# Kernel tuning notes

Measured on AMD Instinct MI355X. Metric: run time of the kernel, lower is better.

## Reference

```python
import jax, jax.numpy as jnp
import numpy as np

EPS = 1e-3  # keras BatchNormalization default epsilon

def hard_sigmoid(x):
    # keras ConvLSTM default recurrent_activation
    return jnp.clip(0.2 * x + 0.5, 0.0, 1.0)

def conv1d(x, w):
    # x: [N, L, Cin], w: [K, Cin, Cout], stride 1, SAME padding
    return jax.lax.conv_general_dilated(x, w, (1,), 'SAME',
                                        dimension_numbers=('NWC', 'WIO', 'NWC'))

def convlstm1d(x, Wx, Wh, b):
    # x: [B, T, L, Cin]; Wx: [3, Cin, 4F]; Wh: [3, F, 4F]; b: [4F]
    # Keras gate order along last axis: i, f, c, o; activation='relu'.
    B, T, L, Cin = x.shape
    F = Wh.shape[1]
    # precompute input-to-gate convs for all timesteps at once
    xg = conv1d(x.reshape(B * T, L, Cin), Wx).reshape(B, T, L, 4 * F) + b

    def step(carry, xg_t):
        h, c = carry  # [B, L, F] each
        g = xg_t + conv1d(h, Wh)          # [B, L, 4F]
        i, f, cg, o = jnp.split(g, 4, axis=-1)
        c = hard_sigmoid(f) * c + hard_sigmoid(i) * jax.nn.relu(cg)
        h = hard_sigmoid(o) * jax.nn.relu(c)
        return (h, c), h

    h0 = jnp.zeros((B, L, F), x.dtype)
    _, hs = jax.lax.scan(step, (h0, h0), jnp.moveaxis(xg, 1, 0))
    return jnp.moveaxis(hs, 0, 1)  # [B, T, L, F]

def bn(x, g, be, m, v):
    # inference-mode BatchNormalization over last (channel) axis
    return (x - m) * jax.lax.rsqrt(v + EPS) * g + be

def setup_inputs() -> dict:
    key = jax.random.key(0)
    ks = iter(jax.random.split(key, 40))
    B, T, L = 32, 32, 128
    F1, F2, F3 = 64, 128, 256
    def w(shape, s=0.05):
        return (s * jax.random.normal(next(ks), shape)).astype(jnp.float32)
    def bn_params(c):
        return (jnp.ones((c,), jnp.float32) + w((c,)), w((c,)),
                w((c,)), jnp.ones((c,), jnp.float32))
    d = {'x': jax.random.normal(next(ks), (B, T, L), jnp.float32)}
    d['Wx1'], d['Wh1'], d['b1'] = w((3, 1, 4 * F1)), w((3, F1, 4 * F1)), w((4 * F1,))
    d['Wx2'], d['Wh2'], d['b2'] = w((3, F1, 4 * F2)), w((3, F2, 4 * F2)), w((4 * F2,))
    d['Wx3'], d['Wh3'], d['b3'] = w((3, F2, 4 * F3)), w((3, F3, 4 * F3)), w((4 * F3,))
    d['g1'], d['be1'], d['m1'], d['v1'] = bn_params(F1)
    d['g2'], d['be2'], d['m2'], d['v2'] = bn_params(F2)
    d['g3'], d['be3'], d['m3'], d['v3'] = bn_params(F3)
    d['D1'], d['db1'] = w((L * F3, 1024), 0.02), w((1024,))
    d['D2'], d['db2'] = w((1024, 512), 0.02), w((512,))
    d['D3'], d['db3'] = w((512, 5), 0.02), w((5,))
    return d

def reference(x, Wx1, Wh1, b1, Wx2, Wh2, b2, Wx3, Wh3, b3,
              g1, be1, m1, v1, g2, be2, m2, v2, g3, be3, m3, v3,
              D1, db1, D2, db2, D3, db3):
    a = x[..., None]                                   # [B, T, L, 1]
    a = bn(convlstm1d(a, Wx1, Wh1, b1), g1, be1, m1, v1)   # [B, T, L, 64]
    a = bn(convlstm1d(a, Wx2, Wh2, b2), g2, be2, m2, v2)   # [B, T, L, 128]
    a = convlstm1d(a, Wx3, Wh3, b3)[:, -1]              # return_sequences=False -> [B, L, 256]
    a = bn(a, g3, be3, m3, v3)
    a = a.reshape(a.shape[0], -1)                       # [B, L*256]
    a = jax.nn.relu(a @ D1 + db1)
    a = jax.nn.relu(a @ D2 + db2)
    return jax.nn.softmax(a @ D3 + db3, axis=-1)        # [B, 5]
```

## Files before the change

### kernel.cpp

```cpp
#include <hip/hip_runtime.h>
#include <math.h>

#define BN_EPS 1e-3f

typedef unsigned short ushort;
typedef unsigned int uint;
typedef __attribute__((ext_vector_type(8))) short bf16x8;
typedef __attribute__((ext_vector_type(4))) float f32x4;

__device__ __forceinline__ float hsig(float x) {
    return fminf(fmaxf(0.2f * x + 0.5f, 0.f), 1.f);
}
__device__ __forceinline__ ushort f2bf(float f) {
    uint u = __float_as_uint(f);
    u += 0x7fffu + ((u >> 16) & 1u);
    return (ushort)(u >> 16);
}

__device__ __forceinline__ void gld_lds16(const void* g, void* l) {
    __builtin_amdgcn_global_load_lds(
        (const __attribute__((address_space(1))) void*)g,
        (__attribute__((address_space(3))) void*)l, 16, 0, 0);
}

__global__ __launch_bounds__(256)
void pack_w(const float* __restrict__ Wx, int Cin,
            const float* __restrict__ Wh, int F,
            uint4* __restrict__ wp, int S0, int S)
{
    __shared__ ushort Wt[32][136];
    const int nblk = blockIdx.x, step = blockIdx.y;
    const int tid = threadIdx.x;
    const int N4 = 4 * F;

    for (int idx = tid; idx < 32 * 128; idx += 256) {
        int kk = idx >> 7, c = idx & 127;
        int gate = c >> 5, fl = c & 31;
        int n = gate * F + nblk * 32 + fl;
        float v = 0.f;
        if (step < S0) {
            int ka = step * 32 + kk;
            if (ka < 3 * Cin) v = Wx[(long)ka * N4 + n];
        } else {
            int ka = (step - S0) * 32 + kk;
            v = Wh[(long)ka * N4 + n];
        }
        Wt[kk][c] = f2bf(v);
    }
    __syncthreads();

    for (int s = tid; s < 512; s += 256) {
        int colgrp = s >> 6, qq = (s >> 4) & 3, rr = s & 15;
        int gate = colgrp >> 1, wn = colgrp & 1;
        int c = gate * 32 + wn * 16 + rr;
        ushort tmp[8];
#pragma unroll
        for (int j = 0; j < 8; ++j) tmp[j] = Wt[qq * 8 + j][c];
        wp[(long)(nblk * S + step) * 512 + s] = *(const uint4*)tmp;
    }
}

struct GateCfg {
    const void* a0;
    const ushort* h_old;
    ushort* h_new;
    const uint4* wp;
    const float* bias;
    float* c_state;
    void* bn_out;
    const float* bn_g; const float* bn_b; const float* bn_m; const float* bn_v;
    long a0_bs;
    long bn_bs;
    int C0, S0, S, F;
    int nf_log2;
    int cin1;
    int bnf32;
    int active;
};

__global__ __launch_bounds__(256)
void gate_diag(GateCfg c3, GateCfg c2, GateCfg c1, int L)
{
    constexpr int ASLOTS = 256;
    constexpr int BSLOTS = 512;

    __shared__ __align__(16) ushort As[2][ASLOTS * 8];
    __shared__ __align__(16) ushort Bs[2][BSLOTS * 8];

    GateCfg c; int tile;
    const int bid = blockIdx.x;
    if (bid < 512)      { c = c3; tile = bid; }
    else if (bid < 768) { c = c2; tile = bid - 512; }
    else                { c = c1; tile = bid - 768; }
    if (!c.active) return;

    const int fblk = tile & ((1 << c.nf_log2) - 1);
    const int rest = tile >> c.nf_log2;
    const int lblk = rest & 1;
    const int b = rest >> 1;

    const int tid = threadIdx.x;
    const int lane = tid & 63;
    const int wave = tid >> 6;
    const int wn = wave & 1, wm = wave >> 1;
    const int q = lane >> 4, r = lane & 15;
    const int f0 = fblk * 32;
    const int l0 = lblk * 64;
    const int F = c.F;
    const int c0shift = 31 - __clz(c.C0 > 0 ? c.C0 : 1);
    const int cFshift = 31 - __clz(F);
    const int S = c.S, S0 = c.S0;

    const int mtile = tid >> 6, within = tid & 63;
    const int qq = within >> 4, rr = within & 15;
    const int row = mtile * 16 + rr;
    const int base_l = l0 + row - 1;

    const ushort* a0p = (const ushort*)c.a0 + (long)b * c.a0_bs
                        + ((long)base_l << c0shift) + qq * 8;
    const ushort* hp  = c.h_old + ((long)b * L + base_l) * F + qq * 8;
    const uint4*  wpB = c.wp + (long)fblk * S * BSLOTS;

    auto a_fetch = [&](int step, uint4& out) {
        out = uint4{0u, 0u, 0u, 0u};
        if (c.cin1 && step < S0) {
            if (qq == 0) {
                const float* xb = (const float*)c.a0 + (long)b * c.a0_bs;
                ushort t[8] = {0, 0, 0, 0, 0, 0, 0, 0};
#pragma unroll
                for (int j = 0; j < 3; ++j) {
                    int l = base_l + j;
                    if (l >= 0 && l < L) t[j] = f2bf(xb[l]);
                }
                out = *(const uint4*)t;
            }
            return;
        }
        const ushort* p; int kb, csh;
        if (step < S0) { p = a0p; kb = step * 32;        csh = c0shift; }
        else           { p = hp;  kb = (step - S0) * 32; csh = cFshift; }
        int l = base_l + (kb >> csh);
        if ((unsigned)l < (unsigned)L) out = *(const uint4*)(p + kb);
    };

    auto b_stage = [&](int step, int bufi) {
        const uint4* src = wpB + (long)step * BSLOTS + tid;
        ushort* dst = &Bs[bufi][(tid & ~63) * 8];
#pragma unroll
        for (int j = 0; j < 2; ++j)
            gld_lds16(src + j * 256, dst + j * 256 * 8);
    };

    f32x4 acc[2][4];
#pragma unroll
    for (int mt = 0; mt < 2; ++mt)
#pragma unroll
        for (int g = 0; g < 4; ++g) acc[mt][g] = (f32x4)(0.f);

    {
        uint4 aP;
        b_stage(0, 0);
        a_fetch(0, aP);
        ((uint4*)As[0])[tid] = aP;
    }
    __syncthreads();

    for (int step = 0; step < S; ++step) {
        const int buf = step & 1;
        const int nbuf = buf ^ 1;
        const bool hasNext = (step + 1 < S);
        uint4 aN;
        if (hasNext) {
            b_stage(step + 1, nbuf);
            a_fetch(step + 1, aN);
        }

        bf16x8 af[2], bfr[4];
#pragma unroll
        for (int mt = 0; mt < 2; ++mt)
            af[mt] = *(const bf16x8*)&As[buf][((wm * 2 + mt) * 64 + lane) * 8];
#pragma unroll
        for (int g = 0; g < 4; ++g)
            bfr[g] = *(const bf16x8*)&Bs[buf][((g * 2 + wn) * 64 + lane) * 8];
#pragma unroll
        for (int mt = 0; mt < 2; ++mt)
#pragma unroll
            for (int g = 0; g < 4; ++g)
                acc[mt][g] = __builtin_amdgcn_mfma_f32_16x16x32_bf16(
                    af[mt], bfr[g], acc[mt][g], 0, 0, 0);

        if (hasNext) ((uint4*)As[nbuf])[tid] = aN;
        __syncthreads();
    }

    const int f = f0 + wn * 16 + r;
    const float b_i = c.bias[f], b_f = c.bias[F + f];
    const float b_c = c.bias[2 * F + f], b_o = c.bias[3 * F + f];
    float sc = 0.f, sh = 0.f;
    if (c.bn_out) {
        sc = c.bn_g[f] * rsqrtf(c.bn_v[f] + BN_EPS);
        sh = c.bn_b[f] - c.bn_m[f] * sc;
    }
#pragma unroll
    for (int mt = 0; mt < 2; ++mt) {
#pragma unroll
        for (int reg = 0; reg < 4; ++reg) {
            const int l = l0 + (wm * 2 + mt) * 16 + q * 4 + reg;
            const long idx = ((long)b * L + l) * F + f;
            float gi = acc[mt][0][reg] + b_i;
            float gf = acc[mt][1][reg] + b_f;
            float gc = acc[mt][2][reg] + b_c;
            float go = acc[mt][3][reg] + b_o;
            float cold = c.c_state[idx];
            float cn = hsig(gf) * cold + hsig(gi) * fmaxf(gc, 0.f);
            float hn = hsig(go) * fmaxf(cn, 0.f);
            c.c_state[idx] = cn;
            c.h_new[idx] = f2bf(hn);
            if (c.bn_out) {
                float bv = hn * sc + sh;
                if (c.bnf32)
                    ((float*)c.bn_out)[(long)b * c.bn_bs + (long)l * F + f] = bv;
                else
                    ((ushort*)c.bn_out)[(long)b * c.bn_bs + (long)l * F + f] = f2bf(bv);
            }
        }
    }
}

#define DP_FMA(kk, W) do {                                         \
    const f32x4 a0 = *(const f32x4*)&A_s[(kk) * 32 + mg * 8];      \
    const f32x4 a1 = *(const f32x4*)&A_s[(kk) * 32 + mg * 8 + 4];  \
    acc[0] += a0.x * (W); acc[1] += a0.y * (W);                    \
    acc[2] += a0.z * (W); acc[3] += a0.w * (W);                    \
    acc[4] += a1.x * (W); acc[5] += a1.y * (W);                    \
    acc[6] += a1.z * (W); acc[7] += a1.w * (W);                    \
} while (0)

__global__ __launch_bounds__(256)
void dense_partial(const float* __restrict__ A,
                   const float* __restrict__ Wt,
                   float* __restrict__ partials,
                   int K, int N)
{
    __shared__ __align__(16) float A_s[128 * 32];
    const int n0 = blockIdx.x * 256;
    const int k0 = blockIdx.y * 128;
    const int tid = threadIdx.x;

    for (int idx = tid; idx < 128 * 32; idx += 256) {
        int k = idx >> 5, m = idx & 31;
        A_s[idx] = A[(long)m * K + k0 + k];
    }
    __syncthreads();

    const int nq = (tid & 63) * 4;
    const int mg = tid >> 6;
    f32x4 acc[8];
#pragma unroll
    for (int i = 0; i < 8; ++i) acc[i] = (f32x4)(0.f);

    const float* wptr = &Wt[(long)k0 * N + n0 + nq];
    f32x4 wcur = *(const f32x4*)wptr;
    f32x4 wnx  = *(const f32x4*)(wptr + N);
    wptr += 2 * (long)N;

#pragma unroll 2
    for (int k = 0; k < 126; ++k) {
        f32x4 wnew = *(const f32x4*)wptr;
        wptr += N;
        DP_FMA(k, wcur);
        wcur = wnx; wnx = wnew;
    }
    DP_FMA(126, wcur);
    DP_FMA(127, wnx);

#pragma unroll
    for (int mm = 0; mm < 8; ++mm)
        *(f32x4*)&partials[((long)blockIdx.y * 32 + mg * 8 + mm) * N + n0 + nq] = acc[mm];
}

__global__ __launch_bounds__(256)
void dense_reduce_relu(const float* __restrict__ partials,
                       const float* __restrict__ bias,
                       float* __restrict__ out, int N, int nK)
{
    int idx = blockIdx.x * 256 + threadIdx.x;
    int m = idx / N, n = idx % N;
    float s = bias[n];
#pragma unroll 4
    for (int j = 0; j < nK; ++j) s += partials[((long)j * 32 + m) * N + n];
    out[idx] = fmaxf(s, 0.f);
}

__global__ __launch_bounds__(256)
void dense_relu(const float* __restrict__ A, const float* __restrict__ Wt,
                const float* __restrict__ bias, float* __restrict__ out,
                int K, int N)
{
    __shared__ float A_s[1024];
    int n = blockIdx.x * 256 + threadIdx.x;
    int m = blockIdx.y;
    for (int k = threadIdx.x; k < K; k += 256) A_s[k] = A[(long)m * K + k];
    __syncthreads();
    float acc = 0.f;
#pragma unroll 8
    for (int k = 0; k < K; ++k)
        acc += A_s[k] * Wt[(long)k * N + n];
    out[(long)m * N + n] = fmaxf(acc + bias[n], 0.f);
}

__global__ __launch_bounds__(64)
void dense_softmax(const float* __restrict__ A, const float* __restrict__ W,
                   const float* __restrict__ bias, float* __restrict__ out)
{
    int b = blockIdx.x;
    int tid = threadIdx.x;
    __shared__ float logits[5];

    float part[5] = {0.f, 0.f, 0.f, 0.f, 0.f};
    for (int k = tid; k < 512; k += 64) {
        float a = A[b * 512 + k];
#pragma unroll
        for (int j = 0; j < 5; ++j) part[j] += a * W[k * 5 + j];
    }
#pragma unroll
    for (int j = 0; j < 5; ++j) {
        float v = part[j];
        for (int off = 32; off; off >>= 1) v += __shfl_down(v, off);
        if (tid == 0) logits[j] = v + bias[j];
    }
    __syncthreads();
    if (tid == 0) {
        float mx = logits[0];
        for (int j = 1; j < 5; ++j) mx = fmaxf(mx, logits[j]);
        float s = 0.f, e[5];
        for (int j = 0; j < 5; ++j) { e[j] = expf(logits[j] - mx); s += e[j]; }
        for (int j = 0; j < 5; ++j) out[b * 5 + j] = e[j] / s;
    }
}

extern "C" void kernel_launch(void* const* d_in, const int* in_sizes, int n_in,
                              void* d_out, int out_size, void* d_ws, size_t ws_size,
                              hipStream_t stream)
{
    const int B = 32, T = 32, L = 128;
    const int F1 = 64, F2 = 128, F3 = 256;

    const float* x   = (const float*)d_in[0];
    const float* Wx1 = (const float*)d_in[1];
    const float* Wh1 = (const float*)d_in[2];
    const float* b1  = (const float*)d_in[3];
    const float* Wx2 = (const float*)d_in[4];
    const float* Wh2 = (const float*)d_in[5];
    const float* b2  = (const float*)d_in[6];
    const float* Wx3 = (const float*)d_in[7];
    const float* Wh3 = (const float*)d_in[8];
    const float* b3  = (const float*)d_in[9];
    const float* g1  = (const float*)d_in[10];
    const float* be1 = (const float*)d_in[11];
    const float* m1  = (const float*)d_in[12];
    const float* v1  = (const float*)d_in[13];
    const float* g2  = (const float*)d_in[14];
    const float* be2 = (const float*)d_in[15];
    const float* m2  = (const float*)d_in[16];
    const float* v2  = (const float*)d_in[17];
    const float* g3  = (const float*)d_in[18];
    const float* be3 = (const float*)d_in[19];
    const float* m3  = (const float*)d_in[20];
    const float* v3  = (const float*)d_in[21];
    const float* D1  = (const float*)d_in[22];
    const float* db1 = (const float*)d_in[23];
    const float* D2  = (const float*)d_in[24];
    const float* db2 = (const float*)d_in[25];
    const float* D3  = (const float*)d_in[26];
    const float* db3 = (const float*)d_in[27];
    (void)in_sizes; (void)n_in; (void)out_size; (void)ws_size;

    char* p = (char*)d_ws;
    ushort* h1seq = (ushort*)p; p += (size_t)B * T * L * F1 * 2;
    ushort* h2seq = (ushort*)p; p += (size_t)B * T * L * F2 * 2;
    ushort* h1a = (ushort*)p; p += (size_t)B * L * F1 * 2;
    ushort* h1b = (ushort*)p; p += (size_t)B * L * F1 * 2;
    ushort* h2a = (ushort*)p; p += (size_t)B * L * F2 * 2;
    ushort* h2b = (ushort*)p; p += (size_t)B * L * F2 * 2;
    ushort* h3a = (ushort*)p; p += (size_t)B * L * F3 * 2;
    ushort* h3b = (ushort*)p; p += (size_t)B * L * F3 * 2;
    float*  c1s = (float*)p; p += (size_t)B * L * F1 * 4;
    float*  c2s = (float*)p; p += (size_t)B * L * F2 * 4;
    float*  c3s = (float*)p; p += (size_t)B * L * F3 * 4;
    float*  h3bn = (float*)p; p += (size_t)B * L * F3 * 4;
    uint4*  wp1 = (uint4*)p; p += (size_t)2 * 7 * 512 * 16;
    uint4*  wp2 = (uint4*)p; p += (size_t)4 * 18 * 512 * 16;
    uint4*  wp3 = (uint4*)p; p += (size_t)8 * 36 * 512 * 16;
    float*  a1 = (float*)p; p += (size_t)B * 1024 * 4;
    float*  a2 = (float*)p; p += (size_t)B * 512 * 4;
    float* partials = (float*)h2seq;

    pack_w<<<dim3(2, 7), 256, 0, stream>>>(Wx1, 1, Wh1, F1, wp1, 1, 7);
    pack_w<<<dim3(4, 18), 256, 0, stream>>>(Wx2, F1, Wh2, F2, wp2, 6, 18);
    pack_w<<<dim3(8, 36), 256, 0, stream>>>(Wx3, F2, Wh3, F3, wp3, 12, 36);

    hipMemsetAsync(h1a, 0, (size_t)B * L * F1 * 2, stream);
    hipMemsetAsync(h2a, 0, (size_t)B * L * F2 * 2, stream);
    hipMemsetAsync(h3a, 0, (size_t)B * L * F3 * 2, stream);
    hipMemsetAsync(c1s, 0, (size_t)B * L * F1 * 4, stream);
    hipMemsetAsync(c2s, 0, (size_t)B * L * F2 * 4, stream);
    hipMemsetAsync(c3s, 0, (size_t)B * L * F3 * 4, stream);

    for (int d = 0; d < T + 2; ++d) {
        GateCfg c1c = {}, c2c = {}, c3c = {};

        int t1 = d;
        if (t1 >= 0 && t1 < T) {
            c1c.active = 1; c1c.cin1 = 1; c1c.bnf32 = 0;
            c1c.a0 = x + (long)t1 * L; c1c.a0_bs = (long)T * L;
            c1c.C0 = 1; c1c.S0 = 1; c1c.S = 7; c1c.F = F1; c1c.nf_log2 = 1;
            c1c.h_old = (t1 & 1) ? h1b : h1a;
            c1c.h_new = (t1 & 1) ? h1a : h1b;
            c1c.wp = wp1; c1c.bias = b1; c1c.c_state = c1s;
            c1c.bn_out = h1seq + (long)t1 * L * F1; c1c.bn_bs = (long)T * L * F1;
            c1c.bn_g = g1; c1c.bn_b = be1; c1c.bn_m = m1; c1c.bn_v = v1;
        }
        int t2 = d - 1;
        if (t2 >= 0 && t2 < T) {
            c2c.active = 1; c2c.cin1 = 0; c2c.bnf32 = 0;
            c2c.a0 = h1seq + (long)t2 * L * F1; c2c.a0_bs = (long)T * L * F1;
            c2c.C0 = F1; c2c.S0 = 6; c2c.S = 18; c2c.F = F2; c2c.nf_log2 = 2;
            c2c.h_old = (t2 & 1) ? h2b : h2a;
            c2c.h_new = (t2 & 1) ? h2a : h2b;
            c2c.wp = wp2; c2c.bias = b2; c2c.c_state = c2s;
            c2c.bn_out = h2seq + (long)t2 * L * F2; c2c.bn_bs = (long)T * L * F2;
            c2c.bn_g = g2; c2c.bn_b = be2; c2c.bn_m = m2; c2c.bn_v = v2;
        }
        int t3 = d - 2;
        if (t3 >= 0 && t3 < T) {
            c3c.active = 1; c3c.cin1 = 0; c3c.bnf32 = 1;
            c3c.a0 = h2seq + (long)t3 * L * F2; c3c.a0_bs = (long)T * L * F2;
            c3c.C0 = F2; c3c.S0 = 12; c3c.S = 36; c3c.F = F3; c3c.nf_log2 = 3;
            c3c.h_old = (t3 & 1) ? h3b : h3a;
            c3c.h_new = (t3 & 1) ? h3a : h3b;
            c3c.wp = wp3; c3c.bias = b3; c3c.c_state = c3s;
            c3c.bn_out = (t3 == T - 1) ? (void*)h3bn : nullptr;
            c3c.bn_bs = (long)L * F3;
            c3c.bn_g = g3; c3c.bn_b = be3; c3c.bn_m = m3; c3c.bn_v = v3;
        }
        gate_diag<<<896, 256, 0, stream>>>(c3c, c2c, c1c, L);
    }

    {
        const int K = L * F3;
        dense_partial<<<dim3(4, 256), 256, 0, stream>>>(h3bn, D1, partials, K, 1024);
        dense_reduce_relu<<<(B * 1024) / 256, 256, 0, stream>>>(partials, db1, a1, 1024, 256);
    }
    dense_relu<<<dim3(512 / 256, B), 256, 0, stream>>>(a1, D2, db2, a2, 1024, 512);
    dense_softmax<<<B, 64, 0, stream>>>(a2, D3, db3, (float*)d_out);
}
```

Before: 1.372 ms.

## Triple-buffer gate GEMM and load A tiles directly to LDS

```diff
diff --git a/kernel.cpp b/kernel.cpp
--- a/kernel.cpp
+++ b/kernel.cpp
@@ -79,13 +79,14 @@
 };
 
 __global__ __launch_bounds__(256)
-void gate_diag(GateCfg c3, GateCfg c2, GateCfg c1, int L)
+void gate_diag(GateCfg c3, GateCfg c2, GateCfg c1, int L,
+               const ushort* __restrict__ zbuf)
 {
     constexpr int ASLOTS = 256;
     constexpr int BSLOTS = 512;
 
-    __shared__ __align__(16) ushort As[2][ASLOTS * 8];
-    __shared__ __align__(16) ushort Bs[2][BSLOTS * 8];
+    __shared__ __align__(16) ushort As[3][ASLOTS * 8];
+    __shared__ __align__(16) ushort Bs[3][BSLOTS * 8];
 
     GateCfg c; int tile;
     const int bid = blockIdx.x;
@@ -111,9 +112,8 @@
     const int cFshift = 31 - __clz(F);
     const int S = c.S, S0 = c.S0;
 
-    const int mtile = tid >> 6, within = tid & 63;
-    const int qq = within >> 4, rr = within & 15;
-    const int row = mtile * 16 + rr;
+    const int qq = lane >> 4, rr = lane & 15;
+    const int row = wave * 16 + rr;
     const int base_l = l0 + row - 1;
 
     const ushort* a0p = (const ushort*)c.a0 + (long)b * c.a0_bs
@@ -121,59 +121,64 @@
     const ushort* hp  = c.h_old + ((long)b * L + base_l) * F + qq * 8;
     const uint4*  wpB = c.wp + (long)fblk * S * BSLOTS;
 
-    auto a_fetch = [&](int step, uint4& out) {
-        out = uint4{0u, 0u, 0u, 0u};
-        if (c.cin1 && step < S0) {
-            if (qq == 0) {
-                const float* xb = (const float*)c.a0 + (long)b * c.a0_bs;
-                ushort t[8] = {0, 0, 0, 0, 0, 0, 0, 0};
-#pragma unroll
-                for (int j = 0; j < 3; ++j) {
-                    int l = base_l + j;
-                    if (l >= 0 && l < L) t[j] = f2bf(xb[l]);
-                }
-                out = *(const uint4*)t;
-            }
-            return;
-        }
+    auto stageB = [&](int step, int bufi) {
+        const uint4* src = wpB + (long)step * BSLOTS + tid;
+        ushort* dst = &Bs[bufi][(tid & ~63) * 8];
+        gld_lds16(src, dst);
+        gld_lds16(src + 256, dst + 256 * 8);
+    };
+    auto stageA = [&](int step, int bufi) {
         const ushort* p; int kb, csh;
         if (step < S0) { p = a0p; kb = step * 32;        csh = c0shift; }
         else           { p = hp;  kb = (step - S0) * 32; csh = cFshift; }
-        int l = base_l + (kb >> csh);
-        if ((unsigned)l < (unsigned)L) out = *(const uint4*)(p + kb);
+        const int l = base_l + (kb >> csh);
+        const void* src = ((unsigned)l < (unsigned)L) ? (const void*)(p + kb)
+                                                      : (const void*)zbuf;
+        gld_lds16(src, &As[bufi][(tid & ~63) * 8]);
     };
 
-    auto b_stage = [&](int step, int bufi) {
-        const uint4* src = wpB + (long)step * BSLOTS + tid;
-        ushort* dst = &Bs[bufi][(tid & ~63) * 8];
-#pragma unroll
-        for (int j = 0; j < 2; ++j)
-            gld_lds16(src + j * 256, dst + j * 256 * 8);
-    };
-
     f32x4 acc[2][4];
 #pragma unroll
     for (int mt = 0; mt < 2; ++mt)
 #pragma unroll
         for (int g = 0; g < 4; ++g) acc[mt][g] = (f32x4)(0.f);
 
-    {
-        uint4 aP;
-        b_stage(0, 0);
-        a_fetch(0, aP);
-        ((uint4*)As[0])[tid] = aP;
-    }
-    __syncthreads();
+    if (c.cin1) {
+        uint4 a0v = {0u, 0u, 0u, 0u};
+        if (qq == 0) {
+            const float* xb = (const float*)c.a0 + (long)b * c.a0_bs;
+            ushort t[8] = {0, 0, 0, 0, 0, 0, 0, 0};
+#pragma unroll
+            for (int j = 0; j < 3; ++j) {
+                int l = base_l + j;
+                if (l >= 0 && l < L) t[j] = f2bf(xb[l]);
+            }
+            a0v = *(const uint4*)t;
+        }
+        ((uint4*)As[0])[tid] = a0v;
+        asm volatile("s_waitcnt lgkmcnt(0)" ::: "memory");
+        stageB(0, 0);
+    } else {
+        stageB(0, 0);
+        stageA(0, 0);
+    }
+    stageB(1, 1);
+    stageA(1, 1);
 
     for (int step = 0; step < S; ++step) {
-        const int buf = step & 1;
-        const int nbuf = buf ^ 1;
-        const bool hasNext = (step + 1 < S);
-        uint4 aN;
-        if (hasNext) {
-            b_stage(step + 1, nbuf);
-            a_fetch(step + 1, aN);
-        }
+        const int buf = step % 3;
+        if (step + 2 < S) {
+            const int nb = (step + 2) % 3;
+            stageB(step + 2, nb);
+            stageA(step + 2, nb);
+            asm volatile("s_waitcnt vmcnt(6)" ::: "memory");
+        } else if (step + 1 < S) {
+            asm volatile("s_waitcnt vmcnt(3)" ::: "memory");
+        } else {
+            asm volatile("s_waitcnt vmcnt(0)" ::: "memory");
+        }
+        __builtin_amdgcn_s_barrier();
+        __builtin_amdgcn_sched_barrier(0);
 
         bf16x8 af[2], bfr[4];
 #pragma unroll
@@ -189,8 +194,8 @@
                 acc[mt][g] = __builtin_amdgcn_mfma_f32_16x16x32_bf16(
                     af[mt], bfr[g], acc[mt][g], 0, 0, 0);
 
-        if (hasNext) ((uint4*)As[nbuf])[tid] = aN;
-        __syncthreads();
+        __builtin_amdgcn_sched_barrier(0);
+        __builtin_amdgcn_s_barrier();
     }
 
     const int f = f0 + wn * 16 + r;
@@ -394,6 +399,7 @@
     uint4*  wp3 = (uint4*)p; p += (size_t)8 * 36 * 512 * 16;
     float*  a1 = (float*)p; p += (size_t)B * 1024 * 4;
     float*  a2 = (float*)p; p += (size_t)B * 512 * 4;
+    ushort* zbuf = (ushort*)p; p += 64;
     float* partials = (float*)h2seq;
 
     pack_w<<<dim3(2, 7), 256, 0, stream>>>(Wx1, 1, Wh1, F1, wp1, 1, 7);
@@ -406,6 +412,7 @@
     hipMemsetAsync(c1s, 0, (size_t)B * L * F1 * 4, stream);
     hipMemsetAsync(c2s, 0, (size_t)B * L * F2 * 4, stream);
     hipMemsetAsync(c3s, 0, (size_t)B * L * F3 * 4, stream);
+    hipMemsetAsync(zbuf, 0, 64, stream);
 
     for (int d = 0; d < T + 2; ++d) {
         GateCfg c1c = {}, c2c = {}, c3c = {};
@@ -444,7 +451,7 @@
             c3c.bn_bs = (long)L * F3;
             c3c.bn_g = g3; c3c.bn_b = be3; c3c.bn_m = m3; c3c.bn_v = v3;
         }
-        gate_diag<<<896, 256, 0, stream>>>(c3c, c2c, c1c, L);
+        gate_diag<<<896, 256, 0, stream>>>(c3c, c2c, c1c, L, zbuf);
     }
 
     {
```

Result: faster. 1.341 ms (-2.3%).

## Stage full input/hidden slab in LDS once, stream weights via registers

Applied to the files above, without the earlier changes.

```diff
diff --git a/kernel.cpp b/kernel.cpp
--- a/kernel.cpp
+++ b/kernel.cpp
@@ -15,12 +15,6 @@
     uint u = __float_as_uint(f);
     u += 0x7fffu + ((u >> 16) & 1u);
     return (ushort)(u >> 16);
-}
-
-__device__ __forceinline__ void gld_lds16(const void* g, void* l) {
-    __builtin_amdgcn_global_load_lds(
-        (const __attribute__((address_space(1))) void*)g,
-        (__attribute__((address_space(3))) void*)l, 16, 0, 0);
 }
 
 __global__ __launch_bounds__(256)
@@ -71,21 +65,19 @@
     const float* bn_g; const float* bn_b; const float* bn_m; const float* bn_v;
     long a0_bs;
     long bn_bs;
-    int C0, S0, S, F;
+    int C0A, S0, S, F;
     int nf_log2;
     int cin1;
     int bnf32;
     int active;
 };
 
+#define MAX_SLAB (66 * 768)
+
 __global__ __launch_bounds__(256)
 void gate_diag(GateCfg c3, GateCfg c2, GateCfg c1, int L)
 {
-    constexpr int ASLOTS = 256;
-    constexpr int BSLOTS = 512;
-
-    __shared__ __align__(16) ushort As[2][ASLOTS * 8];
-    __shared__ __align__(16) ushort Bs[2][BSLOTS * 8];
+    __shared__ __align__(16) char slab[MAX_SLAB];
 
     GateCfg c; int tile;
     const int bid = blockIdx.x;
@@ -107,49 +99,61 @@
     const int f0 = fblk * 32;
     const int l0 = lblk * 64;
     const int F = c.F;
-    const int c0shift = 31 - __clz(c.C0 > 0 ? c.C0 : 1);
+    const int C0A = c.C0A;
+    const int S = c.S, S0 = c.S0;
+    const int c0shift = 31 - __clz(C0A);
     const int cFshift = 31 - __clz(F);
-    const int S = c.S, S0 = c.S0;
-
-    const int mtile = tid >> 6, within = tid & 63;
-    const int qq = within >> 4, rr = within & 15;
-    const int row = mtile * 16 + rr;
-    const int base_l = l0 + row - 1;
-
-    const ushort* a0p = (const ushort*)c.a0 + (long)b * c.a0_bs
-                        + ((long)base_l << c0shift) + qq * 8;
-    const ushort* hp  = c.h_old + ((long)b * L + base_l) * F + qq * 8;
-    const uint4*  wpB = c.wp + (long)fblk * S * BSLOTS;
-
-    auto a_fetch = [&](int step, uint4& out) {
-        out = uint4{0u, 0u, 0u, 0u};
-        if (c.cin1 && step < S0) {
-            if (qq == 0) {
-                const float* xb = (const float*)c.a0 + (long)b * c.a0_bs;
+    const int RS = (C0A + F) * 2;
+    const int NCH = RS >> 4;
+
+    const uint4* wpB = c.wp + (long)fblk * S * 512 + wn * 64 + lane;
+    bf16x8 bA[4], bB[4];
+    auto loadB = [&](int step, bf16x8* bv) {
+#pragma unroll
+        for (int g = 0; g < 4; ++g)
+            bv[g] = *(const bf16x8*)(wpB + (long)step * 512 + g * 128);
+    };
+    loadB(0, bA);
+
+    if (c.cin1) {
+        const float* xb = (const float*)c.a0 + (long)b * c.a0_bs;
+        for (int s = tid; s < 66 * 4; s += 256) {
+            int ri = s >> 2, co = s & 3;
+            uint4 v = {0u, 0u, 0u, 0u};
+            if (co == 0) {
                 ushort t[8] = {0, 0, 0, 0, 0, 0, 0, 0};
 #pragma unroll
                 for (int j = 0; j < 3; ++j) {
-                    int l = base_l + j;
+                    int l = l0 - 1 + ri + j;
                     if (l >= 0 && l < L) t[j] = f2bf(xb[l]);
                 }
-                out = *(const uint4*)t;
+                v = *(const uint4*)t;
             }
-            return;
-        }
-        const ushort* p; int kb, csh;
-        if (step < S0) { p = a0p; kb = step * 32;        csh = c0shift; }
-        else           { p = hp;  kb = (step - S0) * 32; csh = cFshift; }
-        int l = base_l + (kb >> csh);
-        if ((unsigned)l < (unsigned)L) out = *(const uint4*)(p + kb);
-    };
-
-    auto b_stage = [&](int step, int bufi) {
-        const uint4* src = wpB + (long)step * BSLOTS + tid;
-        ushort* dst = &Bs[bufi][(tid & ~63) * 8];
-#pragma unroll
-        for (int j = 0; j < 2; ++j)
-            gld_lds16(src + j * 256, dst + j * 256 * 8);
-    };
+            int ba = (ri * RS + co * 16) ^ ((ri & 7) << 4);
+            *(uint4*)(slab + ba) = v;
+        }
+    }
+    {
+        const ushort* a0b = (const ushort*)c.a0 + (long)b * c.a0_bs;
+        const ushort* hb  = c.h_old + (long)b * L * F;
+        const int c0bytes = C0A * 2;
+        for (int s = tid; s < 66 * NCH; s += 256) {
+            int ri = s / NCH, co = s - ri * NCH;
+            int boff = co * 16;
+            if (c.cin1 && boff < c0bytes) continue;
+            int l = l0 - 1 + ri;
+            uint4 v = {0u, 0u, 0u, 0u};
+            if ((unsigned)l < (unsigned)L) {
+                if (boff >= c0bytes)
+                    v = *(const uint4*)(hb + (long)l * F + ((boff - c0bytes) >> 1));
+                else
+                    v = *(const uint4*)(a0b + (long)l * C0A + (boff >> 1));
+            }
+            int ba = (ri * RS + boff) ^ ((ri & 7) << 4);
+            *(uint4*)(slab + ba) = v;
+        }
+    }
+    __syncthreads();
 
     f32x4 acc[2][4];
 #pragma unroll
@@ -157,41 +161,37 @@
 #pragma unroll
         for (int g = 0; g < 4; ++g) acc[mt][g] = (f32x4)(0.f);
 
-    {
-        uint4 aP;
-        b_stage(0, 0);
-        a_fetch(0, aP);
-        ((uint4*)As[0])[tid] = aP;
-    }
-    __syncthreads();
-
-    for (int step = 0; step < S; ++step) {
-        const int buf = step & 1;
-        const int nbuf = buf ^ 1;
-        const bool hasNext = (step + 1 < S);
-        uint4 aN;
-        if (hasNext) {
-            b_stage(step + 1, nbuf);
-            a_fetch(step + 1, aN);
-        }
-
-        bf16x8 af[2], bfr[4];
-#pragma unroll
-        for (int mt = 0; mt < 2; ++mt)
-            af[mt] = *(const bf16x8*)&As[buf][((wm * 2 + mt) * 64 + lane) * 8];
-#pragma unroll
-        for (int g = 0; g < 4; ++g)
-            bfr[g] = *(const bf16x8*)&Bs[buf][((g * 2 + wn) * 64 + lane) * 8];
+    const int laneoff0 = q * 16;
+
+    auto compute = [&](int step, bf16x8* bv) {
+        int kb, csh, cbyte;
+        if (step < S0) { kb = step * 32;        csh = c0shift; cbyte = 0; }
+        else           { kb = (step - S0) * 32; csh = cFshift; cbyte = C0A * 2; }
+        const int tap = kb >> csh;
+        const int choff = cbyte + ((kb & ((1 << csh) - 1)) << 1) + laneoff0;
+        bf16x8 af[2];
+#pragma unroll
+        for (int mt = 0; mt < 2; ++mt) {
+            int ri = (wm * 2 + mt) * 16 + r + tap;
+            int ba = (ri * RS + choff) ^ ((ri & 7) << 4);
+            af[mt] = *(const bf16x8*)(slab + ba);
+        }
 #pragma unroll
         for (int mt = 0; mt < 2; ++mt)
 #pragma unroll
             for (int g = 0; g < 4; ++g)
                 acc[mt][g] = __builtin_amdgcn_mfma_f32_16x16x32_bf16(
-                    af[mt], bfr[g], acc[mt][g], 0, 0, 0);
-
-        if (hasNext) ((uint4*)As[nbuf])[tid] = aN;
-        __syncthreads();
-    }
+                    af[mt], bv[g], acc[mt][g], 0, 0, 0);
+    };
+
+    int step = 0;
+    for (; step + 2 <= S; step += 2) {
+        loadB(step + 1, bB);
+        compute(step, bA);
+        if (step + 2 < S) loadB(step + 2, bA);
+        compute(step + 1, bB);
+    }
+    if (step < S) compute(step, bA);
 
     const int f = f0 + wn * 16 + r;
     const float b_i = c.bias[f], b_f = c.bias[F + f];
@@ -228,12 +228,11 @@
 }
 
 #define DP_FMA(kk, W) do {                                         \
-    const f32x4 a0 = *(const f32x4*)&A_s[(kk) * 32 + mg * 8];      \
-    const f32x4 a1 = *(const f32x4*)&A_s[(kk) * 32 + mg * 8 + 4];  \
-    acc[0] += a0.x * (W); acc[1] += a0.y * (W);                    \
-    acc[2] += a0.z * (W); acc[3] += a0.w * (W);                    \
-    acc[4] += a1.x * (W); acc[5] += a1.y * (W);                    \
-    acc[6] += a1.z * (W); acc[7] += a1.w * (W);                    \
+    const float* ap = &A_s[(kk) * 33 + mg * 8];                    \
+    acc[0] += ap[0] * (W); acc[1] += ap[1] * (W);                  \
+    acc[2] += ap[2] * (W); acc[3] += ap[3] * (W);                  \
+    acc[4] += ap[4] * (W); acc[5] += ap[5] * (W);                  \
+    acc[6] += ap[6] * (W); acc[7] += ap[7] * (W);                  \
 } while (0)
 
 __global__ __launch_bounds__(256)
@@ -242,14 +241,14 @@
                    float* __restrict__ partials,
                    int K, int N)
 {
-    __shared__ __align__(16) float A_s[128 * 32];
+    __shared__ __align__(16) float A_s[128 * 33];
     const int n0 = blockIdx.x * 256;
     const int k0 = blockIdx.y * 128;
     const int tid = threadIdx.x;
 
     for (int idx = tid; idx < 128 * 32; idx += 256) {
-        int k = idx >> 5, m = idx & 31;
-        A_s[idx] = A[(long)m * K + k0 + k];
+        int m = idx >> 7, kk = idx & 127;
+        A_s[kk * 33 + m] = A[(long)m * K + k0 + kk];
     }
     __syncthreads();
 
@@ -259,20 +258,18 @@
 #pragma unroll
     for (int i = 0; i < 8; ++i) acc[i] = (f32x4)(0.f);
 
-    const float* wptr = &Wt[(long)k0 * N + n0 + nq];
-    f32x4 wcur = *(const f32x4*)wptr;
-    f32x4 wnx  = *(const f32x4*)(wptr + N);
-    wptr += 2 * (long)N;
-
-#pragma unroll 2
-    for (int k = 0; k < 126; ++k) {
-        f32x4 wnew = *(const f32x4*)wptr;
-        wptr += N;
-        DP_FMA(k, wcur);
-        wcur = wnx; wnx = wnew;
-    }
-    DP_FMA(126, wcur);
-    DP_FMA(127, wnx);
+    const float* wp0 = &Wt[(long)k0 * N + n0 + nq];
+#define LDW(kk) (*(const f32x4*)(wp0 + (long)(kk) * N))
+    f32x4 wa = LDW(0), wb = LDW(1), wc = LDW(2), wd = LDW(3);
+
+    for (int k = 0; k < 124; k += 4) {
+        DP_FMA(k + 0, wa); wa = LDW(k + 4);
+        DP_FMA(k + 1, wb); wb = LDW(k + 5);
+        DP_FMA(k + 2, wc); wc = LDW(k + 6);
+        DP_FMA(k + 3, wd); wd = LDW(k + 7);
+    }
+    DP_FMA(124, wa); DP_FMA(125, wb); DP_FMA(126, wc); DP_FMA(127, wd);
+#undef LDW
 
 #pragma unroll
     for (int mm = 0; mm < 8; ++mm)
@@ -414,7 +411,7 @@
         if (t1 >= 0 && t1 < T) {
             c1c.active = 1; c1c.cin1 = 1; c1c.bnf32 = 0;
             c1c.a0 = x + (long)t1 * L; c1c.a0_bs = (long)T * L;
-            c1c.C0 = 1; c1c.S0 = 1; c1c.S = 7; c1c.F = F1; c1c.nf_log2 = 1;
+            c1c.C0A = 32; c1c.S0 = 1; c1c.S = 7; c1c.F = F1; c1c.nf_log2 = 1;
             c1c.h_old = (t1 & 1) ? h1b : h1a;
             c1c.h_new = (t1 & 1) ? h1a : h1b;
             c1c.wp = wp1; c1c.bias = b1; c1c.c_state = c1s;
@@ -425,7 +422,7 @@
         if (t2 >= 0 && t2 < T) {
             c2c.active = 1; c2c.cin1 = 0; c2c.bnf32 = 0;
             c2c.a0 = h1seq + (long)t2 * L * F1; c2c.a0_bs = (long)T * L * F1;
-            c2c.C0 = F1; c2c.S0 = 6; c2c.S = 18; c2c.F = F2; c2c.nf_log2 = 2;
+            c2c.C0A = F1; c2c.S0 = 6; c2c.S = 18; c2c.F = F2; c2c.nf_log2 = 2;
             c2c.h_old = (t2 & 1) ? h2b : h2a;
             c2c.h_new = (t2 & 1) ? h2a : h2b;
             c2c.wp = wp2; c2c.bias = b2; c2c.c_state = c2s;
@@ -436,7 +433,7 @@
         if (t3 >= 0 && t3 < T) {
             c3c.active = 1; c3c.cin1 = 0; c3c.bnf32 = 1;
             c3c.a0 = h2seq + (long)t3 * L * F2; c3c.a0_bs = (long)T * L * F2;
-            c3c.C0 = F2; c3c.S0 = 12; c3c.S = 36; c3c.F = F3; c3c.nf_log2 = 3;
+            c3c.C0A = F2; c3c.S0 = 12; c3c.S = 36; c3c.F = F3; c3c.nf_log2 = 3;
             c3c.h_old = (t3 & 1) ? h3b : h3a;
             c3c.h_new = (t3 & 1) ? h3a : h3b;
             c3c.wp = wp3; c3c.bias = b3; c3c.c_state = c3s;
```

Measured after the change: 1.333 ms. 2.9% less time.
